# Kernel optimization log

Hardware: AMD Instinct MI355X
Metric: run time of the kernel (lower is better)

Reference implementation:

```python
import jax, jax.numpy as jnp
import numpy as np

S, B, V, E, H, C, NV = 256, 64, 50000, 300, 512, 46, 4
EPS = 1e-8


def setup_inputs() -> dict:
    key = jax.random.key(0)
    ks = jax.random.split(key, 17)
    f = lambda i, shape, s=0.05: jax.random.normal(ks[i], shape, jnp.float32) * s
    return {
        "seq": jax.random.randint(ks[0], (S, B), 0, V),
        "emb_table": f(1, (V, E), 1.0),
        "w_ih0": f(2, (4 * H, E)), "w_hh0": f(3, (4 * H, H)),
        "b_ih0": f(4, (4 * H,)), "b_hh0": f(5, (4 * H,)),
        "w_ih1": f(6, (4 * H, H)), "w_hh1": f(7, (4 * H, H)),
        "b_ih1": f(8, (4 * H,)), "b_hh1": f(9, (4 * H,)),
        "lin_w": f(10, (H, H)), "lin_b": f(11, (H,)),
        "out_w": f(12, (C, H)), "out_b": f(13, (C,)),
        "pred_w": f(14, (C, 2 * C)), "pred_b": f(15, (C,)),
        "label_embed": f(16, (C, NV, E), 1.0),
    }


def _lstm_layer(x, w_ih, w_hh, b_ih, b_hh):
    # x: [S, B, in]; PyTorch gate order i, f, g, o
    bsz, hid = x.shape[1], w_hh.shape[1]

    def step(carry, xt):
        h, c = carry
        g = xt @ w_ih.T + h @ w_hh.T + b_ih + b_hh  # [B, 4H]
        i, fg, gg, o = jnp.split(g, 4, axis=-1)
        c = jax.nn.sigmoid(fg) * c + jax.nn.sigmoid(i) * jnp.tanh(gg)
        h = jax.nn.sigmoid(o) * jnp.tanh(c)
        return (h, c), h

    h0 = jnp.zeros((bsz, hid), x.dtype)
    _, hs = jax.lax.scan(step, (h0, h0), x)
    return hs  # [S, B, H]


def reference(seq, emb_table, w_ih0, w_hh0, b_ih0, b_hh0, w_ih1, w_hh1, b_ih1, b_hh1,
              lin_w, lin_b, out_w, out_b, pred_w, pred_b, label_embed):
    embed = emb_table[seq]  # [S, B, E]
    h = _lstm_layer(embed, w_ih0, w_hh0, b_ih0, b_hh0)
    h = _lstm_layer(h, w_ih1, w_hh1, b_ih1, b_hh1)  # dropout inactive (eval)
    feature = h[-1] @ lin_w.T + lin_b               # [B, H]
    lstm_output = feature @ out_w.T + out_b         # [B, C]

    # Batched replacement of the per-label/value cosine-similarity loop:
    # cos[s,b,c,v] = <embed[s,b], label[c,v]> / max(|embed[s,b]|*|label[c,v]|, eps)
    en = jnp.linalg.norm(embed, axis=-1)            # [S, B]
    ln = jnp.linalg.norm(label_embed, axis=-1)      # [C, V]
    num = jnp.einsum('sbe,cve->sbcv', embed, label_embed)
    cos = num / jnp.maximum(en[:, :, None, None] * ln[None, None, :, :], EPS)
    match_input = cos.max(axis=(0, 3))              # max over seq then values -> [B, C]

    x = jnp.concatenate([match_input, lstm_output], axis=1)  # [B, 2C]
    return x @ pred_w.T + pred_b                    # [B, C]
```

## Files before the change

kernel.cpp:

```cpp
#include <hip/hip_runtime.h>
#include <hip/hip_bf16.h>
#include <hip/hip_fp16.h>
#include <math.h>

#define S_LEN 256
#define BATCH 64
#define EMB 300
#define HID 512
#define NCLS 46
#define NVAL 4
#define G4H 2048
#define KPAD 320
#define NPADC 256
#define EPSV 1e-8f

using half8   = __attribute__((ext_vector_type(8))) _Float16;
using floatx4 = __attribute__((ext_vector_type(4))) float;

__device__ __forceinline__ float fsigm(float x) { return 1.f / (1.f + __expf(-x)); }
__device__ __forceinline__ float ftanh(float x) {
    float e2 = __expf(-2.f * x);
    return (1.f - e2) / (1.f + e2);
}
__device__ __forceinline__ float h2f(unsigned short u) {
    union { unsigned short s; _Float16 h; } cv; cv.s = u; return (float)cv.h;
}
__device__ __forceinline__ half8 pack8(const float* p) {
    float4 f0 = *(const float4*)p;
    float4 f1 = *(const float4*)(p + 4);
    half8 h;
    h[0] = (_Float16)f0.x; h[1] = (_Float16)f0.y; h[2] = (_Float16)f0.z; h[3] = (_Float16)f0.w;
    h[4] = (_Float16)f1.x; h[5] = (_Float16)f1.y; h[6] = (_Float16)f1.z; h[7] = (_Float16)f1.w;
    return h;
}

__global__ void k_label_norm(const float* __restrict__ label, float* __restrict__ ln) {
    int r = blockIdx.x;
    int lane = threadIdx.x;
    const float* row = label + (size_t)r * EMB;
    float ss = 0.f;
    for (int e = lane; e < EMB; e += 64) { float v = row[e]; ss += v * v; }
    #pragma unroll
    for (int off = 32; off; off >>= 1) ss += __shfl_down(ss, off);
    if (lane == 0) ln[r] = sqrtf(ss);
}

__global__ __launch_bounds__(256) void k_gather(const int* __restrict__ seq,
                                                const float* __restrict__ emb,
                                                float* __restrict__ embed,
                                                float* __restrict__ en) {
    int p = blockIdx.x * 4 + (threadIdx.x >> 6);
    int lane = threadIdx.x & 63;
    int row = seq[p];
    const float4* src = (const float4*)(emb + (size_t)row * EMB);
    float4* dst = (float4*)(embed + (size_t)p * EMB);
    float ss = 0.f;
    for (int e = lane; e < EMB / 4; e += 64) {
        float4 v = src[e];
        dst[e] = v;
        ss += v.x * v.x + v.y * v.y + v.z * v.z + v.w * v.w;
    }
    #pragma unroll
    for (int off = 32; off; off >>= 1) ss += __shfl_down(ss, off);
    if (lane == 0) en[p] = sqrtf(ss);
}

__global__ __launch_bounds__(256) void k_cvt(const float* __restrict__ in,
                                             unsigned short* __restrict__ out,
                                             int in_rows, int out_rows) {
    int r = blockIdx.x * 4 + (threadIdx.x >> 6);
    if (r >= out_rows) return;
    int lane = threadIdx.x & 63;
    for (int e = lane; e < 80; e += 64) {
        int c = e * 4;
        ushort4 o = {0, 0, 0, 0};
        if (r < in_rows && c < EMB) {
            float4 v = *(const float4*)(in + (size_t)r * EMB + c);
            union { _Float16 h; unsigned short s; } a, b, cc, d;
            a.h = (_Float16)v.x; b.h = (_Float16)v.y; cc.h = (_Float16)v.z; d.h = (_Float16)v.w;
            o.x = a.s; o.y = b.s; o.z = cc.s; o.w = d.s;
        }
        *(ushort4*)(out + (size_t)r * KPAD + c) = o;
    }
}

__global__ __launch_bounds__(256) void k_mkxh(const float* __restrict__ embed,
                                              unsigned short* __restrict__ Xh) {
    int p = blockIdx.x * 4 + (threadIdx.x >> 6);
    int lane = threadIdx.x & 63;
    const float4* src = (const float4*)(embed + (size_t)p * EMB);
    for (int e = lane; e < 80; e += 64) {
        ushort4 o = {0, 0, 0, 0};
        if (e < 75) {
            float4 v = src[e];
            union { _Float16 h; unsigned short s; } a, b, cc, d;
            a.h = (_Float16)v.x; b.h = (_Float16)v.y; cc.h = (_Float16)v.z; d.h = (_Float16)v.w;
            o.x = a.s; o.y = b.s; o.z = cc.s; o.w = d.s;
        }
        *(ushort4*)(Xh + (size_t)p * KPAD + e * 4) = o;
    }
}

template<int OUTF16>
__global__ __launch_bounds__(256) void k_gmm(const unsigned short* __restrict__ X,
                                             const unsigned short* __restrict__ W,
                                             const float* __restrict__ b1,
                                             const float* __restrict__ b2,
                                             void* __restrict__ Yv,
                                             int M, int N) {
    __shared__ __align__(16) char smem[20480];
    unsigned short (*Xs)[40] = (unsigned short(*)[40])smem;
    unsigned short (*Ws)[40] = (unsigned short(*)[40])(smem + 10240);

    int n0 = blockIdx.x * 128, m0 = blockIdx.y * 128;
    int tid = threadIdx.x;
    int w8 = tid >> 6, l = tid & 63, lj = l & 15, q8 = l >> 4;
    int wm = w8 & 1, wn = w8 >> 1;

    floatx4 acc[4][4];
    #pragma unroll
    for (int i = 0; i < 4; i++)
        #pragma unroll
        for (int j = 0; j < 4; j++) acc[i][j] = {0.f, 0.f, 0.f, 0.f};

    for (int k0 = 0; k0 < KPAD; k0 += 32) {
        #pragma unroll
        for (int i = 0; i < 2; i++) {
            int id = i * 256 + tid;
            int r = id >> 2, kc = (id & 3) * 8;
            *(uint4*)&Xs[r][kc] = *(const uint4*)&X[(size_t)(m0 + r) * KPAD + k0 + kc];
            *(uint4*)&Ws[r][kc] = *(const uint4*)&W[(size_t)(n0 + r) * KPAD + k0 + kc];
        }
        __syncthreads();
        half8 A[4], B[4];
        #pragma unroll
        for (int i = 0; i < 4; i++) A[i] = *(const half8*)&Xs[wm * 64 + i * 16 + lj][q8 * 8];
        #pragma unroll
        for (int j = 0; j < 4; j++) B[j] = *(const half8*)&Ws[wn * 64 + j * 16 + lj][q8 * 8];
        #pragma unroll
        for (int i = 0; i < 4; i++)
            #pragma unroll
            for (int j = 0; j < 4; j++)
                acc[i][j] = __builtin_amdgcn_mfma_f32_16x16x32_f16(A[i], B[j], acc[i][j], 0, 0, 0);
        __syncthreads();
    }

    #pragma unroll
    for (int j = 0; j < 4; j++) {
        int col = n0 + wn * 64 + j * 16 + lj;
        float bsum = OUTF16 ? (b1[col] + b2[col]) : 0.f;
        #pragma unroll
        for (int i = 0; i < 4; i++) {
            int row = m0 + wm * 64 + i * 16 + q8 * 4;
            #pragma unroll
            for (int reg = 0; reg < 4; reg++) {
                float v = acc[i][j][reg] + bsum;
                if (OUTF16) {
                    union { _Float16 h; unsigned short s; } cv; cv.h = (_Float16)v;
                    ((unsigned short*)Yv)[(size_t)(row + reg) * N + col] = cv.s;
                } else {
                    ((float*)Yv)[(size_t)(row + reg) * N + col] = v;
                }
            }
        }
    }
}

__global__ __launch_bounds__(256) void k_match(const float* __restrict__ num,
                                               const float* __restrict__ en,
                                               const float* __restrict__ ln,
                                               float* __restrict__ match) {
    int c = blockIdx.x, b = blockIdx.y;
    __shared__ float red[256];
    int s = threadIdx.x;
    float4 nv = *(const float4*)&num[((size_t)s * BATCH + b) * NPADC + c * 4];
    float enb = en[s * BATCH + b];
    float l0 = ln[c * 4 + 0], l1 = ln[c * 4 + 1], l2 = ln[c * 4 + 2], l3 = ln[c * 4 + 3];
    float m = nv.x / fmaxf(enb * l0, EPSV);
    m = fmaxf(m, nv.y / fmaxf(enb * l1, EPSV));
    m = fmaxf(m, nv.z / fmaxf(enb * l2, EPSV));
    m = fmaxf(m, nv.w / fmaxf(enb * l3, EPSV));
    red[s] = m;
    __syncthreads();
    for (int st = 128; st; st >>= 1) {
        if (s < st) red[s] = fmaxf(red[s], red[s + st]);
        __syncthreads();
    }
    if (s == 0) match[b * NCLS + c] = red[0];
}

__global__ __launch_bounds__(512) void k_lstm_pipe(
    const float* __restrict__ w_hh0,
    const unsigned short* __restrict__ G0,
    const float* __restrict__ w_ih1,
    const float* __restrict__ w_hh1,
    const float* __restrict__ b_ih1,
    const float* __restrict__ b_hh1,
    unsigned short* __restrict__ ring0,
    unsigned short* __restrict__ ring1,
    float* __restrict__ hlast,
    int* __restrict__ flags0,
    int* __restrict__ flags1)
{
    __shared__ __align__(16) char smem_raw[24576];
    int bid = blockIdx.x;
    int g = bid & 7;
    int tid = threadIdx.x;
    int w8 = tid >> 6, l = tid & 63, lj = l & 15, q8 = l >> 4;

    if (bid < 64) {
        int r = bid >> 3;
        _Float16 (*hl)[520] = (_Float16(*)[520])smem_raw;
        float (*gbuf)[260] = (float(*)[260])(smem_raw + 8320);

        half8 B0[16], B1[16];
        {
            int lc0 = w8 * 32 + lj;
            int lc1 = w8 * 32 + 16 + lj;
            int wr0 = (lc0 >> 6) * 512 + r * 64 + (lc0 & 63);
            int wr1 = (lc1 >> 6) * 512 + r * 64 + (lc1 & 63);
            #pragma unroll
            for (int kk = 0; kk < 16; kk++) {
                B0[kk] = pack8(w_hh0 + (size_t)wr0 * 512 + kk * 32 + q8 * 8);
                B1[kk] = pack8(w_hh0 + (size_t)wr1 * 512 + kk * 32 + q8 * 8);
            }
        }
        int gb_ = tid >> 6, gj = tid & 63;
        float cst = 0.f;

        for (int t = 0; t < S_LEN; t++) {
            const unsigned short* Gp = G0 + ((size_t)t * BATCH + g * 8 + gb_) * G4H + r * 64 + gj;
            float gv0 = h2f(Gp[0]), gv1 = h2f(Gp[512]), gv2 = h2f(Gp[1024]), gv3 = h2f(Gp[1536]);

            floatx4 acc0 = {0.f, 0.f, 0.f, 0.f}, acc1 = {0.f, 0.f, 0.f, 0.f};
            if (t > 0) {
                if (tid < 8) {
                    int gd = 1 << 20;
                    while (__hip_atomic_load(flags0 + g * 8 + tid, __ATOMIC_RELAXED,
                                             __HIP_MEMORY_SCOPE_AGENT) < t && --gd)
                        __builtin_amdgcn_s_sleep(1);
                }
                __syncthreads();
                {
                    int sb = tid >> 6, sk = (tid & 63) * 8;
                    const unsigned long long* src = (const unsigned long long*)
                        (ring0 + ((size_t)(t - 1) * BATCH + g * 8 + sb) * HID + sk);
                    unsigned long long v0 = __hip_atomic_load(src,     __ATOMIC_RELAXED, __HIP_MEMORY_SCOPE_AGENT);
                    unsigned long long v1 = __hip_atomic_load(src + 1, __ATOMIC_RELAXED, __HIP_MEMORY_SCOPE_AGENT);
                    *(unsigned long long*)&hl[sb][sk]     = v0;
                    *(unsigned long long*)&hl[sb][sk + 4] = v1;
                }
                __syncthreads();
                #pragma unroll
                for (int kk = 0; kk < 16; kk++) {
                    half8 A = *(const half8*)&hl[l & 7][kk * 32 + q8 * 8];
                    acc0 = __builtin_amdgcn_mfma_f32_16x16x32_f16(A, B0[kk], acc0, 0, 0, 0);
                    acc1 = __builtin_amdgcn_mfma_f32_16x16x32_f16(A, B1[kk], acc1, 0, 0, 0);
                }
                if (l < 32) {
                    #pragma unroll
                    for (int ri = 0; ri < 4; ri++) {
                        int row = q8 * 4 + ri;
                        gbuf[row][w8 * 32 + lj]      = acc0[ri];
                        gbuf[row][w8 * 32 + 16 + lj] = acc1[ri];
                    }
                }
                __syncthreads();
            }

            float s_i = gv0 + (t ? gbuf[gb_][gj]       : 0.f);
            float s_f = gv1 + (t ? gbuf[gb_][64 + gj]  : 0.f);
            float s_g = gv2 + (t ? gbuf[gb_][128 + gj] : 0.f);
            float s_o = gv3 + (t ? gbuf[gb_][192 + gj] : 0.f);
            cst = fsigm(s_f) * cst + fsigm(s_i) * ftanh(s_g);
            float hv = fsigm(s_o) * ftanh(cst);

            union { unsigned short s; _Float16 h; } cv; cv.h = (_Float16)hv;
            unsigned int mine = cv.s;
            unsigned int other = (unsigned int)__shfl_xor((int)mine, 1);
            if (!(gj & 1)) {
                unsigned int pk = (mine & 0xFFFFu) | (other << 16);
                unsigned int* rp = (unsigned int*)ring0;
                __hip_atomic_store(rp + (((size_t)t * BATCH + g * 8 + gb_) * HID + r * 64 + gj) / 2,
                                   pk, __ATOMIC_RELAXED, __HIP_MEMORY_SCOPE_AGENT);
            }
            __syncthreads();
            if (tid == 0)
                __hip_atomic_store(flags0 + g * 8 + r, t + 1, __ATOMIC_RELAXED, __HIP_MEMORY_SCOPE_AGENT);
        }
    } else {
        int rid = (bid - 64) >> 3;
        _Float16 (*hl0)[520] = (_Float16(*)[520])smem_raw;
        _Float16 (*hl1)[520] = (_Float16(*)[520])(smem_raw + 8320);
        float (*gbuf)[132] = (float(*)[132])(smem_raw + 16640);

        half8 Bin[16], Brec[16];
        {
            int gate = w8 >> 1;
            int wrow = gate * 512 + rid * 32 + (w8 & 1) * 16 + lj;
            #pragma unroll
            for (int kk = 0; kk < 16; kk++) {
                Bin[kk]  = pack8(w_ih1 + (size_t)wrow * 512 + kk * 32 + q8 * 8);
                Brec[kk] = pack8(w_hh1 + (size_t)wrow * 512 + kk * 32 + q8 * 8);
            }
        }
        float bi = 0.f, bf = 0.f, bgg = 0.f, bo = 0.f;
        if (tid < 256) {
            int u = tid & 31;
            int base = rid * 32 + u;
            bi  = b_ih1[base]        + b_hh1[base];
            bf  = b_ih1[512 + base]  + b_hh1[512 + base];
            bgg = b_ih1[1024 + base] + b_hh1[1024 + base];
            bo  = b_ih1[1536 + base] + b_hh1[1536 + base];
        }
        float cst = 0.f;

        for (int t = 0; t < S_LEN; t++) {
            if (tid < 8) {
                int gd = 1 << 20;
                while (__hip_atomic_load(flags0 + g * 8 + tid, __ATOMIC_RELAXED,
                                         __HIP_MEMORY_SCOPE_AGENT) < t + 1 && --gd)
                    __builtin_amdgcn_s_sleep(1);
            } else if (tid < 24 && t > 0) {
                int gd = 1 << 20;
                while (__hip_atomic_load(flags1 + g * 16 + (tid - 8), __ATOMIC_RELAXED,
                                         __HIP_MEMORY_SCOPE_AGENT) < t && --gd)
                    __builtin_amdgcn_s_sleep(1);
            }
            __syncthreads();

            {
                int sb = tid >> 6, sk = (tid & 63) * 8;
                const unsigned long long* s0 = (const unsigned long long*)
                    (ring0 + ((size_t)t * BATCH + g * 8 + sb) * HID + sk);
                unsigned long long v0 = __hip_atomic_load(s0,     __ATOMIC_RELAXED, __HIP_MEMORY_SCOPE_AGENT);
                unsigned long long v1 = __hip_atomic_load(s0 + 1, __ATOMIC_RELAXED, __HIP_MEMORY_SCOPE_AGENT);
                *(unsigned long long*)&hl0[sb][sk]     = v0;
                *(unsigned long long*)&hl0[sb][sk + 4] = v1;
                if (t > 0) {
                    const unsigned long long* s1 = (const unsigned long long*)
                        (ring1 + ((size_t)(t - 1) * BATCH + g * 8 + sb) * HID + sk);
                    unsigned long long u0 = __hip_atomic_load(s1,     __ATOMIC_RELAXED, __HIP_MEMORY_SCOPE_AGENT);
                    unsigned long long u1 = __hip_atomic_load(s1 + 1, __ATOMIC_RELAXED, __HIP_MEMORY_SCOPE_AGENT);
                    *(unsigned long long*)&hl1[sb][sk]     = u0;
                    *(unsigned long long*)&hl1[sb][sk + 4] = u1;
                }
            }
            __syncthreads();

            floatx4 accA = {0.f, 0.f, 0.f, 0.f}, accB = {0.f, 0.f, 0.f, 0.f};
            #pragma unroll
            for (int kk = 0; kk < 16; kk++) {
                half8 A0 = *(const half8*)&hl0[l & 7][kk * 32 + q8 * 8];
                accA = __builtin_amdgcn_mfma_f32_16x16x32_f16(A0, Bin[kk], accA, 0, 0, 0);
            }
            if (t > 0) {
                #pragma unroll
                for (int kk = 0; kk < 16; kk++) {
                    half8 A1 = *(const half8*)&hl1[l & 7][kk * 32 + q8 * 8];
                    accB = __builtin_amdgcn_mfma_f32_16x16x32_f16(A1, Brec[kk], accB, 0, 0, 0);
                }
            }
            if (l < 32) {
                #pragma unroll
                for (int ri = 0; ri < 4; ri++) {
                    int row = q8 * 4 + ri;
                    gbuf[row][w8 * 16 + lj] = accA[ri] + accB[ri];
                }
            }
            __syncthreads();

            if (tid < 256) {
                int b = tid >> 5, u = tid & 31;
                float s_i = gbuf[b][u]      + bi;
                float s_f = gbuf[b][32 + u] + bf;
                float s_g = gbuf[b][64 + u] + bgg;
                float s_o = gbuf[b][96 + u] + bo;
                cst = fsigm(s_f) * cst + fsigm(s_i) * ftanh(s_g);
                float hv = fsigm(s_o) * ftanh(cst);

                union { unsigned short s; _Float16 h; } cv; cv.h = (_Float16)hv;
                unsigned int mine = cv.s;
                unsigned int other = (unsigned int)__shfl_xor((int)mine, 1);
                if (!(u & 1)) {
                    unsigned int pk = (mine & 0xFFFFu) | (other << 16);
                    unsigned int* rp = (unsigned int*)ring1;
                    __hip_atomic_store(rp + (((size_t)t * BATCH + g * 8 + b) * HID + rid * 32 + u) / 2,
                                       pk, __ATOMIC_RELAXED, __HIP_MEMORY_SCOPE_AGENT);
                }
                if (t == S_LEN - 1)
                    hlast[(g * 8 + b) * HID + rid * 32 + u] = hv;
            }
            __syncthreads();
            if (tid == 0)
                __hip_atomic_store(flags1 + g * 16 + rid, t + 1, __ATOMIC_RELAXED, __HIP_MEMORY_SCOPE_AGENT);
        }
    }
}

__global__ void k_small(const float* __restrict__ X, const float* __restrict__ W,
                        const float* __restrict__ bias, float* __restrict__ Y,
                        int N, int K) {
    int m = blockIdx.x;
    int n = blockIdx.y * 64 + threadIdx.x;
    if (n >= N) return;
    const float* x = X + (size_t)m * K;
    const float* w = W + (size_t)n * K;
    float s = bias[n];
    for (int k = 0; k < K; k++) s += x[k] * w[k];
    Y[(size_t)m * N + n] = s;
}

__global__ void k_final(const float* __restrict__ match, const float* __restrict__ lout,
                        const float* __restrict__ W, const float* __restrict__ bias,
                        float* __restrict__ out) {
    int m = blockIdx.x;
    int n = threadIdx.x;
    if (n >= NCLS) return;
    const float* w = W + (size_t)n * (2 * NCLS);
    float s = bias[n];
    for (int k = 0; k < NCLS; k++) s += match[m * NCLS + k] * w[k];
    for (int k = 0; k < NCLS; k++) s += lout[m * NCLS + k] * w[NCLS + k];
    out[m * NCLS + n] = s;
}

extern "C" void kernel_launch(void* const* d_in, const int* in_sizes, int n_in,
                              void* d_out, int out_size, void* d_ws, size_t ws_size,
                              hipStream_t stream) {
    (void)in_sizes; (void)n_in; (void)out_size; (void)ws_size;
    const int*   seq    = (const int*)d_in[0];
    const float* emb    = (const float*)d_in[1];
    const float* w_ih0  = (const float*)d_in[2];
    const float* w_hh0  = (const float*)d_in[3];
    const float* b_ih0  = (const float*)d_in[4];
    const float* b_hh0  = (const float*)d_in[5];
    const float* w_ih1  = (const float*)d_in[6];
    const float* w_hh1  = (const float*)d_in[7];
    const float* b_ih1  = (const float*)d_in[8];
    const float* b_hh1  = (const float*)d_in[9];
    const float* lin_w  = (const float*)d_in[10];
    const float* lin_b  = (const float*)d_in[11];
    const float* out_w  = (const float*)d_in[12];
    const float* out_b  = (const float*)d_in[13];
    const float* pred_w = (const float*)d_in[14];
    const float* pred_b = (const float*)d_in[15];
    const float* label  = (const float*)d_in[16];

    const int M = S_LEN * BATCH;
    float* ws = (float*)d_ws;
    size_t o = 0;
    float* embed = ws + o; o += (size_t)M * EMB;
    unsigned short* G0 = (unsigned short*)(ws + o); o += (size_t)M * G4H / 2;
    unsigned short* ring0 = (unsigned short*)(ws + o); o += (size_t)M * HID / 2;
    unsigned short* ring1 = (unsigned short*)(ws + o); o += (size_t)M * HID / 2;
    float* h1last = ws + o; o += (size_t)BATCH * HID;
    float* en    = ws + o; o += M;
    float* ln    = ws + o; o += 256;
    float* match = ws + o; o += 3072;
    float* feat  = ws + o; o += (size_t)BATCH * HID;
    float* lout  = ws + o; o += 3072;
    int*   flags0 = (int*)(ws + o); o += 64;
    int*   flags1 = (int*)(ws + o); o += 128;
    unsigned short* Xh  = (unsigned short*)(ws + o); o += (size_t)M * KPAD / 2;
    unsigned short* Lh  = (unsigned short*)(ws + o); o += (size_t)NPADC * KPAD / 2;
    unsigned short* Wh0 = (unsigned short*)(ws + o); o += (size_t)G4H * KPAD / 2;
    float* numG  = ws + o; o += (size_t)M * NPADC;

    hipMemsetAsync(flags0, 0, 192 * sizeof(int), stream);

    k_label_norm<<<NCLS * NVAL, 64, 0, stream>>>(label, ln);
    k_gather<<<M / 4, 256, 0, stream>>>(seq, emb, embed, en);

    k_cvt<<<64, 256, 0, stream>>>(label, Lh, NCLS * NVAL, NPADC);
    k_cvt<<<512, 256, 0, stream>>>(w_ih0, Wh0, G4H, G4H);
    k_mkxh<<<M / 4, 256, 0, stream>>>(embed, Xh);

    k_gmm<0><<<dim3(NPADC / 128, M / 128), 256, 0, stream>>>(Xh, Lh, nullptr, nullptr, numG, M, NPADC);
    k_match<<<dim3(NCLS, BATCH), 256, 0, stream>>>(numG, en, ln, match);

    k_gmm<1><<<dim3(G4H / 128, M / 128), 256, 0, stream>>>(Xh, Wh0, b_ih0, b_hh0, G0, M, G4H);

    k_lstm_pipe<<<192, 512, 0, stream>>>(w_hh0, G0, w_ih1, w_hh1, b_ih1, b_hh1,
                                         ring0, ring1, h1last, flags0, flags1);

    k_small<<<dim3(BATCH, HID / 64), 64, 0, stream>>>(h1last, lin_w, lin_b, feat, HID, HID);
    k_small<<<dim3(BATCH, 1), 64, 0, stream>>>(feat, out_w, out_b, lout, NCLS, HID);
    k_final<<<BATCH, 64, 0, stream>>>(match, lout, pred_w, pred_b, (float*)d_out);
}
```

Before: 1.003 ms.

## Fuse both LSTM layers into one wavefront-skewed persistent kernel with shared flags

```diff
diff --git a/kernel.cpp b/kernel.cpp
--- a/kernel.cpp
+++ b/kernel.cpp
@@ -189,7 +189,7 @@
     if (s == 0) match[b * NCLS + c] = red[0];
 }
 
-__global__ __launch_bounds__(512) void k_lstm_pipe(
+__global__ __launch_bounds__(512, 1) void k_lstm_fused(
     const float* __restrict__ w_hh0,
     const unsigned short* __restrict__ G0,
     const float* __restrict__ w_ih1,
@@ -199,131 +199,55 @@
     unsigned short* __restrict__ ring0,
     unsigned short* __restrict__ ring1,
     float* __restrict__ hlast,
-    int* __restrict__ flags0,
-    int* __restrict__ flags1)
+    int* __restrict__ flags)
 {
-    __shared__ __align__(16) char smem_raw[24576];
+    __shared__ __align__(16) char smem_raw[25088];
+    _Float16 (*hl0)[520] = (_Float16(*)[520])smem_raw;
+    _Float16 (*hl1)[520] = (_Float16(*)[520])(smem_raw + 8320);
+    float (*gbuf0)[132] = (float(*)[132])(smem_raw + 16640);
+    float (*gbuf1)[132] = (float(*)[132])(smem_raw + 20864);
+
     int bid = blockIdx.x;
-    int g = bid & 7;
+    int g = bid & 7, r = bid >> 3;
     int tid = threadIdx.x;
     int w8 = tid >> 6, l = tid & 63, lj = l & 15, q8 = l >> 4;
 
-    if (bid < 64) {
-        int r = bid >> 3;
-        _Float16 (*hl)[520] = (_Float16(*)[520])smem_raw;
-        float (*gbuf)[260] = (float(*)[260])(smem_raw + 8320);
-
-        half8 B0[16], B1[16];
-        {
-            int lc0 = w8 * 32 + lj;
-            int lc1 = w8 * 32 + 16 + lj;
-            int wr0 = (lc0 >> 6) * 512 + r * 64 + (lc0 & 63);
-            int wr1 = (lc1 >> 6) * 512 + r * 64 + (lc1 & 63);
-            #pragma unroll
-            for (int kk = 0; kk < 16; kk++) {
-                B0[kk] = pack8(w_hh0 + (size_t)wr0 * 512 + kk * 32 + q8 * 8);
-                B1[kk] = pack8(w_hh0 + (size_t)wr1 * 512 + kk * 32 + q8 * 8);
-            }
-        }
-        int gb_ = tid >> 6, gj = tid & 63;
-        float cst = 0.f;
-
-        for (int t = 0; t < S_LEN; t++) {
-            const unsigned short* Gp = G0 + ((size_t)t * BATCH + g * 8 + gb_) * G4H + r * 64 + gj;
-            float gv0 = h2f(Gp[0]), gv1 = h2f(Gp[512]), gv2 = h2f(Gp[1024]), gv3 = h2f(Gp[1536]);
-
-            floatx4 acc0 = {0.f, 0.f, 0.f, 0.f}, acc1 = {0.f, 0.f, 0.f, 0.f};
-            if (t > 0) {
-                if (tid < 8) {
-                    int gd = 1 << 20;
-                    while (__hip_atomic_load(flags0 + g * 8 + tid, __ATOMIC_RELAXED,
-                                             __HIP_MEMORY_SCOPE_AGENT) < t && --gd)
-                        __builtin_amdgcn_s_sleep(1);
-                }
-                __syncthreads();
-                {
-                    int sb = tid >> 6, sk = (tid & 63) * 8;
-                    const unsigned long long* src = (const unsigned long long*)
-                        (ring0 + ((size_t)(t - 1) * BATCH + g * 8 + sb) * HID + sk);
-                    unsigned long long v0 = __hip_atomic_load(src,     __ATOMIC_RELAXED, __HIP_MEMORY_SCOPE_AGENT);
-                    unsigned long long v1 = __hip_atomic_load(src + 1, __ATOMIC_RELAXED, __HIP_MEMORY_SCOPE_AGENT);
-                    *(unsigned long long*)&hl[sb][sk]     = v0;
-                    *(unsigned long long*)&hl[sb][sk + 4] = v1;
-                }
-                __syncthreads();
-                #pragma unroll
-                for (int kk = 0; kk < 16; kk++) {
-                    half8 A = *(const half8*)&hl[l & 7][kk * 32 + q8 * 8];
-                    acc0 = __builtin_amdgcn_mfma_f32_16x16x32_f16(A, B0[kk], acc0, 0, 0, 0);
-                    acc1 = __builtin_amdgcn_mfma_f32_16x16x32_f16(A, B1[kk], acc1, 0, 0, 0);
-                }
-                if (l < 32) {
-                    #pragma unroll
-                    for (int ri = 0; ri < 4; ri++) {
-                        int row = q8 * 4 + ri;
-                        gbuf[row][w8 * 32 + lj]      = acc0[ri];
-                        gbuf[row][w8 * 32 + 16 + lj] = acc1[ri];
-                    }
-                }
-                __syncthreads();
-            }
-
-            float s_i = gv0 + (t ? gbuf[gb_][gj]       : 0.f);
-            float s_f = gv1 + (t ? gbuf[gb_][64 + gj]  : 0.f);
-            float s_g = gv2 + (t ? gbuf[gb_][128 + gj] : 0.f);
-            float s_o = gv3 + (t ? gbuf[gb_][192 + gj] : 0.f);
-            cst = fsigm(s_f) * cst + fsigm(s_i) * ftanh(s_g);
-            float hv = fsigm(s_o) * ftanh(cst);
-
-            union { unsigned short s; _Float16 h; } cv; cv.h = (_Float16)hv;
-            unsigned int mine = cv.s;
-            unsigned int other = (unsigned int)__shfl_xor((int)mine, 1);
-            if (!(gj & 1)) {
-                unsigned int pk = (mine & 0xFFFFu) | (other << 16);
-                unsigned int* rp = (unsigned int*)ring0;
-                __hip_atomic_store(rp + (((size_t)t * BATCH + g * 8 + gb_) * HID + r * 64 + gj) / 2,
-                                   pk, __ATOMIC_RELAXED, __HIP_MEMORY_SCOPE_AGENT);
-            }
-            __syncthreads();
-            if (tid == 0)
-                __hip_atomic_store(flags0 + g * 8 + r, t + 1, __ATOMIC_RELAXED, __HIP_MEMORY_SCOPE_AGENT);
-        }
-    } else {
-        int rid = (bid - 64) >> 3;
-        _Float16 (*hl0)[520] = (_Float16(*)[520])smem_raw;
-        _Float16 (*hl1)[520] = (_Float16(*)[520])(smem_raw + 8320);
-        float (*gbuf)[132] = (float(*)[132])(smem_raw + 16640);
-
-        half8 Bin[16], Brec[16];
-        {
-            int gate = w8 >> 1;
-            int wrow = gate * 512 + rid * 32 + (w8 & 1) * 16 + lj;
-            #pragma unroll
-            for (int kk = 0; kk < 16; kk++) {
-                Bin[kk]  = pack8(w_ih1 + (size_t)wrow * 512 + kk * 32 + q8 * 8);
-                Brec[kk] = pack8(w_hh1 + (size_t)wrow * 512 + kk * 32 + q8 * 8);
-            }
-        }
-        float bi = 0.f, bf = 0.f, bgg = 0.f, bo = 0.f;
-        if (tid < 256) {
-            int u = tid & 31;
-            int base = rid * 32 + u;
-            bi  = b_ih1[base]        + b_hh1[base];
-            bf  = b_ih1[512 + base]  + b_hh1[512 + base];
-            bgg = b_ih1[1024 + base] + b_hh1[1024 + base];
-            bo  = b_ih1[1536 + base] + b_hh1[1536 + base];
-        }
-        float cst = 0.f;
-
-        for (int t = 0; t < S_LEN; t++) {
-            if (tid < 8) {
+    half8 B0[16], Bin[16], Brec[16];
+    {
+        int gate = w8 >> 1;
+        int wrow = gate * 512 + r * 32 + (w8 & 1) * 16 + lj;
+        #pragma unroll
+        for (int kk = 0; kk < 16; kk++) {
+            B0[kk]   = pack8(w_hh0 + (size_t)wrow * 512 + kk * 32 + q8 * 8);
+            Bin[kk]  = pack8(w_ih1 + (size_t)wrow * 512 + kk * 32 + q8 * 8);
+            Brec[kk] = pack8(w_hh1 + (size_t)wrow * 512 + kk * 32 + q8 * 8);
+        }
+    }
+    int pb = tid >> 5, pu = tid & 31;
+    float bi = 0.f, bf = 0.f, bgg = 0.f, bo = 0.f;
+    if (tid < 256) {
+        int base = r * 32 + pu;
+        bi  = b_ih1[base]        + b_hh1[base];
+        bf  = b_ih1[512 + base]  + b_hh1[512 + base];
+        bgg = b_ih1[1024 + base] + b_hh1[1024 + base];
+        bo  = b_ih1[1536 + base] + b_hh1[1536 + base];
+    }
+    float c0 = 0.f, c1 = 0.f;
+
+    for (int t = 0; t <= S_LEN; t++) {
+        float gv0 = 0.f, gv1 = 0.f, gv2 = 0.f, gv3 = 0.f;
+        if (t < S_LEN && tid < 256) {
+            const unsigned short* Gp = G0 + ((size_t)t * BATCH + g * 8 + pb) * G4H + r * 32 + pu;
+            gv0 = h2f(Gp[0]); gv1 = h2f(Gp[512]); gv2 = h2f(Gp[1024]); gv3 = h2f(Gp[1536]);
+        }
+
+        floatx4 acc0 = {0.f, 0.f, 0.f, 0.f};
+        floatx4 accI = {0.f, 0.f, 0.f, 0.f};
+        floatx4 accR = {0.f, 0.f, 0.f, 0.f};
+        if (t > 0) {
+            if (tid < 16) {
                 int gd = 1 << 20;
-                while (__hip_atomic_load(flags0 + g * 8 + tid, __ATOMIC_RELAXED,
-                                         __HIP_MEMORY_SCOPE_AGENT) < t + 1 && --gd)
-                    __builtin_amdgcn_s_sleep(1);
-            } else if (tid < 24 && t > 0) {
-                int gd = 1 << 20;
-                while (__hip_atomic_load(flags1 + g * 16 + (tid - 8), __ATOMIC_RELAXED,
+                while (__hip_atomic_load(flags + g * 16 + tid, __ATOMIC_RELAXED,
                                          __HIP_MEMORY_SCOPE_AGENT) < t && --gd)
                     __builtin_amdgcn_s_sleep(1);
             }
@@ -332,14 +256,14 @@
             {
                 int sb = tid >> 6, sk = (tid & 63) * 8;
                 const unsigned long long* s0 = (const unsigned long long*)
-                    (ring0 + ((size_t)t * BATCH + g * 8 + sb) * HID + sk);
+                    (ring0 + ((size_t)(t - 1) * BATCH + g * 8 + sb) * HID + sk);
                 unsigned long long v0 = __hip_atomic_load(s0,     __ATOMIC_RELAXED, __HIP_MEMORY_SCOPE_AGENT);
                 unsigned long long v1 = __hip_atomic_load(s0 + 1, __ATOMIC_RELAXED, __HIP_MEMORY_SCOPE_AGENT);
                 *(unsigned long long*)&hl0[sb][sk]     = v0;
                 *(unsigned long long*)&hl0[sb][sk + 4] = v1;
-                if (t > 0) {
+                if (t > 1) {
                     const unsigned long long* s1 = (const unsigned long long*)
-                        (ring1 + ((size_t)(t - 1) * BATCH + g * 8 + sb) * HID + sk);
+                        (ring1 + ((size_t)(t - 2) * BATCH + g * 8 + sb) * HID + sk);
                     unsigned long long u0 = __hip_atomic_load(s1,     __ATOMIC_RELAXED, __HIP_MEMORY_SCOPE_AGENT);
                     unsigned long long u1 = __hip_atomic_load(s1 + 1, __ATOMIC_RELAXED, __HIP_MEMORY_SCOPE_AGENT);
                     *(unsigned long long*)&hl1[sb][sk]     = u0;
@@ -348,53 +272,73 @@
             }
             __syncthreads();
 
-            floatx4 accA = {0.f, 0.f, 0.f, 0.f}, accB = {0.f, 0.f, 0.f, 0.f};
             #pragma unroll
             for (int kk = 0; kk < 16; kk++) {
                 half8 A0 = *(const half8*)&hl0[l & 7][kk * 32 + q8 * 8];
-                accA = __builtin_amdgcn_mfma_f32_16x16x32_f16(A0, Bin[kk], accA, 0, 0, 0);
-            }
-            if (t > 0) {
+                acc0 = __builtin_amdgcn_mfma_f32_16x16x32_f16(A0, B0[kk],  acc0, 0, 0, 0);
+                accI = __builtin_amdgcn_mfma_f32_16x16x32_f16(A0, Bin[kk], accI, 0, 0, 0);
+            }
+            if (t > 1) {
                 #pragma unroll
                 for (int kk = 0; kk < 16; kk++) {
                     half8 A1 = *(const half8*)&hl1[l & 7][kk * 32 + q8 * 8];
-                    accB = __builtin_amdgcn_mfma_f32_16x16x32_f16(A1, Brec[kk], accB, 0, 0, 0);
+                    accR = __builtin_amdgcn_mfma_f32_16x16x32_f16(A1, Brec[kk], accR, 0, 0, 0);
                 }
             }
             if (l < 32) {
                 #pragma unroll
                 for (int ri = 0; ri < 4; ri++) {
                     int row = q8 * 4 + ri;
-                    gbuf[row][w8 * 16 + lj] = accA[ri] + accB[ri];
+                    gbuf0[row][w8 * 16 + lj] = acc0[ri];
+                    gbuf1[row][w8 * 16 + lj] = accI[ri] + accR[ri];
                 }
             }
             __syncthreads();
-
-            if (tid < 256) {
-                int b = tid >> 5, u = tid & 31;
-                float s_i = gbuf[b][u]      + bi;
-                float s_f = gbuf[b][32 + u] + bf;
-                float s_g = gbuf[b][64 + u] + bgg;
-                float s_o = gbuf[b][96 + u] + bo;
-                cst = fsigm(s_f) * cst + fsigm(s_i) * ftanh(s_g);
-                float hv = fsigm(s_o) * ftanh(cst);
-
+        }
+
+        if (tid < 256) {
+            if (t < S_LEN) {
+                float s_i = gv0 + (t ? gbuf0[pb][pu]       : 0.f);
+                float s_f = gv1 + (t ? gbuf0[pb][32 + pu]  : 0.f);
+                float s_g = gv2 + (t ? gbuf0[pb][64 + pu]  : 0.f);
+                float s_o = gv3 + (t ? gbuf0[pb][96 + pu]  : 0.f);
+                c0 = fsigm(s_f) * c0 + fsigm(s_i) * ftanh(s_g);
+                float hv = fsigm(s_o) * ftanh(c0);
                 union { unsigned short s; _Float16 h; } cv; cv.h = (_Float16)hv;
                 unsigned int mine = cv.s;
                 unsigned int other = (unsigned int)__shfl_xor((int)mine, 1);
-                if (!(u & 1)) {
+                if (!(pu & 1)) {
                     unsigned int pk = (mine & 0xFFFFu) | (other << 16);
-                    unsigned int* rp = (unsigned int*)ring1;
-                    __hip_atomic_store(rp + (((size_t)t * BATCH + g * 8 + b) * HID + rid * 32 + u) / 2,
+                    unsigned int* rp = (unsigned int*)ring0;
+                    __hip_atomic_store(rp + (((size_t)t * BATCH + g * 8 + pb) * HID + r * 32 + pu) / 2,
                                        pk, __ATOMIC_RELAXED, __HIP_MEMORY_SCOPE_AGENT);
                 }
-                if (t == S_LEN - 1)
-                    hlast[(g * 8 + b) * HID + rid * 32 + u] = hv;
-            }
-            __syncthreads();
-            if (tid == 0)
-                __hip_atomic_store(flags1 + g * 16 + rid, t + 1, __ATOMIC_RELAXED, __HIP_MEMORY_SCOPE_AGENT);
-        }
+            }
+            if (t > 0) {
+                float s_i = gbuf1[pb][pu]      + bi;
+                float s_f = gbuf1[pb][32 + pu] + bf;
+                float s_g = gbuf1[pb][64 + pu] + bgg;
+                float s_o = gbuf1[pb][96 + pu] + bo;
+                c1 = fsigm(s_f) * c1 + fsigm(s_i) * ftanh(s_g);
+                float hv = fsigm(s_o) * ftanh(c1);
+                if (t == S_LEN) {
+                    hlast[(g * 8 + pb) * HID + r * 32 + pu] = hv;
+                } else {
+                    union { unsigned short s; _Float16 h; } cv; cv.h = (_Float16)hv;
+                    unsigned int mine = cv.s;
+                    unsigned int other = (unsigned int)__shfl_xor((int)mine, 1);
+                    if (!(pu & 1)) {
+                        unsigned int pk = (mine & 0xFFFFu) | (other << 16);
+                        unsigned int* rp = (unsigned int*)ring1;
+                        __hip_atomic_store(rp + (((size_t)(t - 1) * BATCH + g * 8 + pb) * HID + r * 32 + pu) / 2,
+                                           pk, __ATOMIC_RELAXED, __HIP_MEMORY_SCOPE_AGENT);
+                    }
+                }
+            }
+        }
+        __syncthreads();
+        if (tid == 0 && t < S_LEN)
+            __hip_atomic_store(flags + g * 16 + r, t + 1, __ATOMIC_RELAXED, __HIP_MEMORY_SCOPE_AGENT);
     }
 }
 
@@ -459,14 +403,13 @@
     float* match = ws + o; o += 3072;
     float* feat  = ws + o; o += (size_t)BATCH * HID;
     float* lout  = ws + o; o += 3072;
-    int*   flags0 = (int*)(ws + o); o += 64;
-    int*   flags1 = (int*)(ws + o); o += 128;
+    int*   flags = (int*)(ws + o); o += 128;
     unsigned short* Xh  = (unsigned short*)(ws + o); o += (size_t)M * KPAD / 2;
     unsigned short* Lh  = (unsigned short*)(ws + o); o += (size_t)NPADC * KPAD / 2;
     unsigned short* Wh0 = (unsigned short*)(ws + o); o += (size_t)G4H * KPAD / 2;
     float* numG  = ws + o; o += (size_t)M * NPADC;
 
-    hipMemsetAsync(flags0, 0, 192 * sizeof(int), stream);
+    hipMemsetAsync(flags, 0, 128 * sizeof(int), stream);
 
     k_label_norm<<<NCLS * NVAL, 64, 0, stream>>>(label, ln);
     k_gather<<<M / 4, 256, 0, stream>>>(seq, emb, embed, en);
@@ -480,8 +423,8 @@
 
     k_gmm<1><<<dim3(G4H / 128, M / 128), 256, 0, stream>>>(Xh, Wh0, b_ih0, b_hh0, G0, M, G4H);
 
-    k_lstm_pipe<<<192, 512, 0, stream>>>(w_hh0, G0, w_ih1, w_hh1, b_ih1, b_hh1,
-                                         ring0, ring1, h1last, flags0, flags1);
+    k_lstm_fused<<<128, 512, 0, stream>>>(w_hh0, G0, w_ih1, w_hh1, b_ih1, b_hh1,
+                                          ring0, ring1, h1last, flags);
 
     k_small<<<dim3(BATCH, HID / 64), 64, 0, stream>>>(h1last, lin_w, lin_b, feat, HID, HID);
     k_small<<<dim3(BATCH, 1), 64, 0, stream>>>(feat, out_w, out_b, lout, NCLS, HID);
```

After: 1.087 ms. +8.3%, slower.

## Double LSTM pipeline block size to split per-step MFMA chains across 16 waves

Applied to the files above, without the earlier changes.

```diff
diff --git a/kernel.cpp b/kernel.cpp
--- a/kernel.cpp
+++ b/kernel.cpp
@@ -189,7 +189,7 @@
     if (s == 0) match[b * NCLS + c] = red[0];
 }
 
-__global__ __launch_bounds__(512) void k_lstm_pipe(
+__global__ __launch_bounds__(1024) void k_lstm_pipe(
     const float* __restrict__ w_hh0,
     const unsigned short* __restrict__ G0,
     const float* __restrict__ w_ih1,
@@ -202,37 +202,34 @@
     int* __restrict__ flags0,
     int* __restrict__ flags1)
 {
-    __shared__ __align__(16) char smem_raw[24576];
+    __shared__ __align__(16) char smem_raw[25088];
     int bid = blockIdx.x;
     int g = bid & 7;
     int tid = threadIdx.x;
-    int w8 = tid >> 6, l = tid & 63, lj = l & 15, q8 = l >> 4;
+    int w16 = tid >> 6, l = tid & 63, lj = l & 15, q8 = l >> 4;
 
     if (bid < 64) {
         int r = bid >> 3;
         _Float16 (*hl)[520] = (_Float16(*)[520])smem_raw;
         float (*gbuf)[260] = (float(*)[260])(smem_raw + 8320);
 
-        half8 B0[16], B1[16];
+        half8 B0[16];
         {
-            int lc0 = w8 * 32 + lj;
-            int lc1 = w8 * 32 + 16 + lj;
-            int wr0 = (lc0 >> 6) * 512 + r * 64 + (lc0 & 63);
-            int wr1 = (lc1 >> 6) * 512 + r * 64 + (lc1 & 63);
+            int gate = w16 >> 2;
+            int wrow = gate * 512 + r * 64 + (w16 & 3) * 16 + lj;
             #pragma unroll
-            for (int kk = 0; kk < 16; kk++) {
-                B0[kk] = pack8(w_hh0 + (size_t)wr0 * 512 + kk * 32 + q8 * 8);
-                B1[kk] = pack8(w_hh0 + (size_t)wr1 * 512 + kk * 32 + q8 * 8);
-            }
-        }
-        int gb_ = tid >> 6, gj = tid & 63;
-        float cst = 0.f;
+            for (int kk = 0; kk < 16; kk++)
+                B0[kk] = pack8(w_hh0 + (size_t)wrow * 512 + kk * 32 + q8 * 8);
+        }
+        int pb = tid >> 6, pu = tid & 63;
+        float c0 = 0.f;
 
         for (int t = 0; t < S_LEN; t++) {
-            const unsigned short* Gp = G0 + ((size_t)t * BATCH + g * 8 + gb_) * G4H + r * 64 + gj;
-            float gv0 = h2f(Gp[0]), gv1 = h2f(Gp[512]), gv2 = h2f(Gp[1024]), gv3 = h2f(Gp[1536]);
-
-            floatx4 acc0 = {0.f, 0.f, 0.f, 0.f}, acc1 = {0.f, 0.f, 0.f, 0.f};
+            float gv0 = 0.f, gv1 = 0.f, gv2 = 0.f, gv3 = 0.f;
+            if (tid < 512) {
+                const unsigned short* Gp = G0 + ((size_t)t * BATCH + g * 8 + pb) * G4H + r * 64 + pu;
+                gv0 = h2f(Gp[0]); gv1 = h2f(Gp[512]); gv2 = h2f(Gp[1024]); gv3 = h2f(Gp[1536]);
+            }
             if (t > 0) {
                 if (tid < 8) {
                     int gd = 1 << 20;
@@ -241,7 +238,7 @@
                         __builtin_amdgcn_s_sleep(1);
                 }
                 __syncthreads();
-                {
+                if (tid < 512) {
                     int sb = tid >> 6, sk = (tid & 63) * 8;
                     const unsigned long long* src = (const unsigned long long*)
                         (ring0 + ((size_t)(t - 1) * BATCH + g * 8 + sb) * HID + sk);
@@ -251,38 +248,36 @@
                     *(unsigned long long*)&hl[sb][sk + 4] = v1;
                 }
                 __syncthreads();
+                floatx4 acc = {0.f, 0.f, 0.f, 0.f};
                 #pragma unroll
                 for (int kk = 0; kk < 16; kk++) {
                     half8 A = *(const half8*)&hl[l & 7][kk * 32 + q8 * 8];
-                    acc0 = __builtin_amdgcn_mfma_f32_16x16x32_f16(A, B0[kk], acc0, 0, 0, 0);
-                    acc1 = __builtin_amdgcn_mfma_f32_16x16x32_f16(A, B1[kk], acc1, 0, 0, 0);
+                    acc = __builtin_amdgcn_mfma_f32_16x16x32_f16(A, B0[kk], acc, 0, 0, 0);
                 }
                 if (l < 32) {
                     #pragma unroll
-                    for (int ri = 0; ri < 4; ri++) {
-                        int row = q8 * 4 + ri;
-                        gbuf[row][w8 * 32 + lj]      = acc0[ri];
-                        gbuf[row][w8 * 32 + 16 + lj] = acc1[ri];
-                    }
+                    for (int ri = 0; ri < 4; ri++)
+                        gbuf[q8 * 4 + ri][w16 * 16 + lj] = acc[ri];
                 }
                 __syncthreads();
             }
 
-            float s_i = gv0 + (t ? gbuf[gb_][gj]       : 0.f);
-            float s_f = gv1 + (t ? gbuf[gb_][64 + gj]  : 0.f);
-            float s_g = gv2 + (t ? gbuf[gb_][128 + gj] : 0.f);
-            float s_o = gv3 + (t ? gbuf[gb_][192 + gj] : 0.f);
-            cst = fsigm(s_f) * cst + fsigm(s_i) * ftanh(s_g);
-            float hv = fsigm(s_o) * ftanh(cst);
-
-            union { unsigned short s; _Float16 h; } cv; cv.h = (_Float16)hv;
-            unsigned int mine = cv.s;
-            unsigned int other = (unsigned int)__shfl_xor((int)mine, 1);
-            if (!(gj & 1)) {
-                unsigned int pk = (mine & 0xFFFFu) | (other << 16);
-                unsigned int* rp = (unsigned int*)ring0;
-                __hip_atomic_store(rp + (((size_t)t * BATCH + g * 8 + gb_) * HID + r * 64 + gj) / 2,
-                                   pk, __ATOMIC_RELAXED, __HIP_MEMORY_SCOPE_AGENT);
+            if (tid < 512) {
+                float s_i = gv0 + (t ? gbuf[pb][pu]        : 0.f);
+                float s_f = gv1 + (t ? gbuf[pb][64 + pu]   : 0.f);
+                float s_g = gv2 + (t ? gbuf[pb][128 + pu]  : 0.f);
+                float s_o = gv3 + (t ? gbuf[pb][192 + pu]  : 0.f);
+                c0 = fsigm(s_f) * c0 + fsigm(s_i) * ftanh(s_g);
+                float hv = fsigm(s_o) * ftanh(c0);
+                union { unsigned short s; _Float16 h; } cv; cv.h = (_Float16)hv;
+                unsigned int mine = cv.s;
+                unsigned int other = (unsigned int)__shfl_xor((int)mine, 1);
+                if (!(pu & 1)) {
+                    unsigned int pk = (mine & 0xFFFFu) | (other << 16);
+                    unsigned int* rp = (unsigned int*)ring0;
+                    __hip_atomic_store(rp + (((size_t)t * BATCH + g * 8 + pb) * HID + r * 64 + pu) / 2,
+                                       pk, __ATOMIC_RELAXED, __HIP_MEMORY_SCOPE_AGENT);
+                }
             }
             __syncthreads();
             if (tid == 0)
@@ -292,28 +287,30 @@
         int rid = (bid - 64) >> 3;
         _Float16 (*hl0)[520] = (_Float16(*)[520])smem_raw;
         _Float16 (*hl1)[520] = (_Float16(*)[520])(smem_raw + 8320);
-        float (*gbuf)[132] = (float(*)[132])(smem_raw + 16640);
-
-        half8 Bin[16], Brec[16];
+        float (*gbufI)[132] = (float(*)[132])(smem_raw + 16640);
+        float (*gbufR)[132] = (float(*)[132])(smem_raw + 20864);
+
+        half8 Bw[16];
+        int halfsel = w16 >> 3;
         {
-            int gate = w8 >> 1;
-            int wrow = gate * 512 + rid * 32 + (w8 & 1) * 16 + lj;
+            int tile = w16 & 7;
+            int gate = tile >> 1;
+            int wrow = gate * 512 + rid * 32 + (tile & 1) * 16 + lj;
+            const float* wsrc = halfsel ? w_hh1 : w_ih1;
             #pragma unroll
-            for (int kk = 0; kk < 16; kk++) {
-                Bin[kk]  = pack8(w_ih1 + (size_t)wrow * 512 + kk * 32 + q8 * 8);
-                Brec[kk] = pack8(w_hh1 + (size_t)wrow * 512 + kk * 32 + q8 * 8);
-            }
-        }
+            for (int kk = 0; kk < 16; kk++)
+                Bw[kk] = pack8(wsrc + (size_t)wrow * 512 + kk * 32 + q8 * 8);
+        }
+        int pb = (tid >> 5) & 7, pu = tid & 31;
         float bi = 0.f, bf = 0.f, bgg = 0.f, bo = 0.f;
         if (tid < 256) {
-            int u = tid & 31;
-            int base = rid * 32 + u;
+            int base = rid * 32 + pu;
             bi  = b_ih1[base]        + b_hh1[base];
             bf  = b_ih1[512 + base]  + b_hh1[512 + base];
             bgg = b_ih1[1024 + base] + b_hh1[1024 + base];
             bo  = b_ih1[1536 + base] + b_hh1[1536 + base];
         }
-        float cst = 0.f;
+        float c1 = 0.f;
 
         for (int t = 0; t < S_LEN; t++) {
             if (tid < 8) {
@@ -329,7 +326,7 @@
             }
             __syncthreads();
 
-            {
+            if (tid < 512) {
                 int sb = tid >> 6, sk = (tid & 63) * 8;
                 const unsigned long long* s0 = (const unsigned long long*)
                     (ring0 + ((size_t)t * BATCH + g * 8 + sb) * HID + sk);
@@ -337,59 +334,61 @@
                 unsigned long long v1 = __hip_atomic_load(s0 + 1, __ATOMIC_RELAXED, __HIP_MEMORY_SCOPE_AGENT);
                 *(unsigned long long*)&hl0[sb][sk]     = v0;
                 *(unsigned long long*)&hl0[sb][sk + 4] = v1;
-                if (t > 0) {
-                    const unsigned long long* s1 = (const unsigned long long*)
-                        (ring1 + ((size_t)(t - 1) * BATCH + g * 8 + sb) * HID + sk);
-                    unsigned long long u0 = __hip_atomic_load(s1,     __ATOMIC_RELAXED, __HIP_MEMORY_SCOPE_AGENT);
-                    unsigned long long u1 = __hip_atomic_load(s1 + 1, __ATOMIC_RELAXED, __HIP_MEMORY_SCOPE_AGENT);
-                    *(unsigned long long*)&hl1[sb][sk]     = u0;
-                    *(unsigned long long*)&hl1[sb][sk + 4] = u1;
-                }
+            } else if (t > 0) {
+                int st_ = tid - 512;
+                int sb = st_ >> 6, sk = (st_ & 63) * 8;
+                const unsigned long long* s1 = (const unsigned long long*)
+                    (ring1 + ((size_t)(t - 1) * BATCH + g * 8 + sb) * HID + sk);
+                unsigned long long u0 = __hip_atomic_load(s1,     __ATOMIC_RELAXED, __HIP_MEMORY_SCOPE_AGENT);
+                unsigned long long u1 = __hip_atomic_load(s1 + 1, __ATOMIC_RELAXED, __HIP_MEMORY_SCOPE_AGENT);
+                *(unsigned long long*)&hl1[sb][sk]     = u0;
+                *(unsigned long long*)&hl1[sb][sk + 4] = u1;
             }
             __syncthreads();
 
-            floatx4 accA = {0.f, 0.f, 0.f, 0.f}, accB = {0.f, 0.f, 0.f, 0.f};
-            #pragma unroll
-            for (int kk = 0; kk < 16; kk++) {
-                half8 A0 = *(const half8*)&hl0[l & 7][kk * 32 + q8 * 8];
-                accA = __builtin_amdgcn_mfma_f32_16x16x32_f16(A0, Bin[kk], accA, 0, 0, 0);
-            }
-            if (t > 0) {
+            floatx4 acc = {0.f, 0.f, 0.f, 0.f};
+            if (halfsel == 0) {
+                #pragma unroll
+                for (int kk = 0; kk < 16; kk++) {
+                    half8 A0 = *(const half8*)&hl0[l & 7][kk * 32 + q8 * 8];
+                    acc = __builtin_amdgcn_mfma_f32_16x16x32_f16(A0, Bw[kk], acc, 0, 0, 0);
+                }
+            } else if (t > 0) {
                 #pragma unroll
                 for (int kk = 0; kk < 16; kk++) {
                     half8 A1 = *(const half8*)&hl1[l & 7][kk * 32 + q8 * 8];
-                    accB = __builtin_amdgcn_mfma_f32_16x16x32_f16(A1, Brec[kk], accB, 0, 0, 0);
+                    acc = __builtin_amdgcn_mfma_f32_16x16x32_f16(A1, Bw[kk], acc, 0, 0, 0);
                 }
             }
             if (l < 32) {
+                int tile = w16 & 7;
+                float (*gb)[132] = halfsel ? gbufR : gbufI;
                 #pragma unroll
-                for (int ri = 0; ri < 4; ri++) {
-                    int row = q8 * 4 + ri;
-                    gbuf[row][w8 * 16 + lj] = accA[ri] + accB[ri];
-                }
+                for (int ri = 0; ri < 4; ri++)
+                    gb[q8 * 4 + ri][tile * 16 + lj] = acc[ri];
             }
             __syncthreads();
 
             if (tid < 256) {
-                int b = tid >> 5, u = tid & 31;
-                float s_i = gbuf[b][u]      + bi;
-                float s_f = gbuf[b][32 + u] + bf;
-                float s_g = gbuf[b][64 + u] + bgg;
-                float s_o = gbuf[b][96 + u] + bo;
-                cst = fsigm(s_f) * cst + fsigm(s_i) * ftanh(s_g);
-                float hv = fsigm(s_o) * ftanh(cst);
-
-                union { unsigned short s; _Float16 h; } cv; cv.h = (_Float16)hv;
-                unsigned int mine = cv.s;
-                unsigned int other = (unsigned int)__shfl_xor((int)mine, 1);
-                if (!(u & 1)) {
-                    unsigned int pk = (mine & 0xFFFFu) | (other << 16);
-                    unsigned int* rp = (unsigned int*)ring1;
-                    __hip_atomic_store(rp + (((size_t)t * BATCH + g * 8 + b) * HID + rid * 32 + u) / 2,
-                                       pk, __ATOMIC_RELAXED, __HIP_MEMORY_SCOPE_AGENT);
-                }
-                if (t == S_LEN - 1)
-                    hlast[(g * 8 + b) * HID + rid * 32 + u] = hv;
+                float s_i = gbufI[pb][pu]      + gbufR[pb][pu]      + bi;
+                float s_f = gbufI[pb][32 + pu] + gbufR[pb][32 + pu] + bf;
+                float s_g = gbufI[pb][64 + pu] + gbufR[pb][64 + pu] + bgg;
+                float s_o = gbufI[pb][96 + pu] + gbufR[pb][96 + pu] + bo;
+                c1 = fsigm(s_f) * c1 + fsigm(s_i) * ftanh(s_g);
+                float hv = fsigm(s_o) * ftanh(c1);
+                if (t == S_LEN - 1) {
+                    hlast[(g * 8 + pb) * HID + rid * 32 + pu] = hv;
+                } else {
+                    union { unsigned short s; _Float16 h; } cv; cv.h = (_Float16)hv;
+                    unsigned int mine = cv.s;
+                    unsigned int other = (unsigned int)__shfl_xor((int)mine, 1);
+                    if (!(pu & 1)) {
+                        unsigned int pk = (mine & 0xFFFFu) | (other << 16);
+                        unsigned int* rp = (unsigned int*)ring1;
+                        __hip_atomic_store(rp + (((size_t)t * BATCH + g * 8 + pb) * HID + rid * 32 + pu) / 2,
+                                           pk, __ATOMIC_RELAXED, __HIP_MEMORY_SCOPE_AGENT);
+                    }
+                }
             }
             __syncthreads();
             if (tid == 0)
@@ -480,8 +479,8 @@
 
     k_gmm<1><<<dim3(G4H / 128, M / 128), 256, 0, stream>>>(Xh, Wh0, b_ih0, b_hh0, G0, M, G4H);
 
-    k_lstm_pipe<<<192, 512, 0, stream>>>(w_hh0, G0, w_ih1, w_hh1, b_ih1, b_hh1,
-                                         ring0, ring1, h1last, flags0, flags1);
+    k_lstm_pipe<<<192, 1024, 0, stream>>>(w_hh0, G0, w_ih1, w_hh1, b_ih1, b_hh1,
+                                          ring0, ring1, h1last, flags0, flags1);
 
     k_small<<<dim3(BATCH, HID / 64), 64, 0, stream>>>(h1last, lin_w, lin_b, feat, HID, HID);
     k_small<<<dim3(BATCH, 1), 64, 0, stream>>>(feat, out_w, out_b, lout, NCLS, HID);
```

Measured after the change: 1.047 ms. 1.04x slower.
